# Performance work log

Measured on AMD Instinct MI355X. Metric: run time of the kernel, lower is better.

## Reference

```python
import jax, jax.numpy as jnp
import numpy as np


def _rnn_scan(x_tbi, h0, Wih, Whh, bih, bhh):
    # x_tbi: [T,B,I], h0: [B,H]. PyTorch nn.RNN cell: h = tanh(x@Wih^T + bih + h@Whh^T + bhh)
    def step(h, xt):
        h_new = jnp.tanh(xt @ Wih.T + bih + h @ Whh.T + bhh)
        return h_new, h_new
    h_last, hs = jax.lax.scan(step, h0, x_tbi)
    return h_last, hs


def setup_inputs() -> dict:
    key = jax.random.key(0)
    ks = jax.random.split(key, 12)
    B, T, I, H, O = 4096, 64, 3, 128, 3
    s = 1.0 / np.sqrt(H)
    d = {
        "x": jax.random.normal(ks[0], (B, T, I), dtype=jnp.float32),
        "enc_Wih": jax.random.uniform(ks[1], (H, I), jnp.float32, -s, s),
        "enc_Whh": jax.random.uniform(ks[2], (H, H), jnp.float32, -s, s),
        "enc_bih": jax.random.uniform(ks[3], (H,), jnp.float32, -s, s),
        "enc_bhh": jax.random.uniform(ks[4], (H,), jnp.float32, -s, s),
        "dec_Wih": jax.random.uniform(ks[5], (H, O), jnp.float32, -s, s),
        "dec_Whh": jax.random.uniform(ks[6], (H, H), jnp.float32, -s, s),
        "dec_bih": jax.random.uniform(ks[7], (H,), jnp.float32, -s, s),
        "dec_bhh": jax.random.uniform(ks[8], (H,), jnp.float32, -s, s),
        "fc_W": jax.random.uniform(ks[9], (O, H), jnp.float32, -s, s),
        "fc_b": jax.random.uniform(ks[10], (O,), jnp.float32, -s, s),
        "pred_len": 32,
    }
    return d


def reference(x, enc_Wih, enc_Whh, enc_bih, enc_bhh,
              dec_Wih, dec_Whh, dec_bih, dec_bhh, fc_W, fc_b, pred_len):
    B, T, _ = x.shape
    H = enc_Whh.shape[0]
    h0 = jnp.zeros((B, H), dtype=x.dtype)
    # Encoder over LOOK_BACK steps
    h, _ = _rnn_scan(jnp.swapaxes(x, 0, 1), h0, enc_Wih, enc_Whh, enc_bih, enc_bhh)
    dec_in0 = x[:, -1, :]  # [B,O]

    def step(carry, _):
        h, inp = carry
        h_new = jnp.tanh(inp @ dec_Wih.T + dec_bih + h @ dec_Whh.T + dec_bhh)
        pred = h_new @ fc_W.T + fc_b
        return (h_new, pred), pred

    _, preds = jax.lax.scan(step, (h, dec_in0), None, length=pred_len)
    out = jnp.swapaxes(preds, 0, 1)  # [B, pred_len, O]
    if pred_len == 1:
        return out[:, 0, :]
    return out
```

## Files before the change

### kernel.cpp

```cpp
#include <hip/hip_runtime.h>

typedef short short8 __attribute__((ext_vector_type(8)));
typedef float f32x4 __attribute__((ext_vector_type(4)));

#define H 128
#define NB 16
#define TSTEPS 64
#define PRED 32


static __device__ __forceinline__ unsigned short bf16_rne(float f) {
  unsigned u = __builtin_bit_cast(unsigned, f);
  u += 0x7fffu + ((u >> 16) & 1u);
  return (unsigned short)(u >> 16);
}
static __device__ __forceinline__ float bf16_f(unsigned short s) {
  unsigned u = ((unsigned)s) << 16;
  return __builtin_bit_cast(float, u);
}
static __device__ __forceinline__ float tanh_fast(float v) {
  v = fminf(9.0f, fmaxf(-9.0f, v));
  float e = __expf(2.0f * v);
  return __fdividef(e - 1.0f, e + 1.0f);
}

static __device__ __forceinline__ void split_frag(const f32x4& a, const f32x4& b,
                                                  short8& hi, short8& lo) {
  #pragma unroll
  for (int e = 0; e < 4; ++e) {
    unsigned short h1 = bf16_rne(a[e]);
    hi[e] = (short)h1;
    lo[e] = (short)bf16_rne(a[e] - bf16_f(h1));
    unsigned short h2 = bf16_rne(b[e]);
    hi[e + 4] = (short)h2;
    lo[e + 4] = (short)bf16_rne(b[e] - bf16_f(h2));
  }
}

__global__ __launch_bounds__(512, 2) void traj_kernel(
    const float* __restrict__ x,
    const float* __restrict__ eWih, const float* __restrict__ eWhh,
    const float* __restrict__ ebih, const float* __restrict__ ebhh,
    const float* __restrict__ dWih, const float* __restrict__ dWhh,
    const float* __restrict__ dbih, const float* __restrict__ dbhh,
    const float* __restrict__ fcW, const float* __restrict__ fcb,
    float* __restrict__ out)
{
  __shared__ __align__(16) short h_hi0[NB * H];
  __shared__ __align__(16) short h_hi1[NB * H];

  const int tid = threadIdx.x;
  const int lane = tid & 63;
  const int w = tid >> 6;
  const int l4 = lane >> 4;
  const int ln = lane & 15;
  const int r0 = blockIdx.x * NB;
  const int jj = w * 16 + ln;

  #pragma unroll
  for (int s = 0; s < 4; ++s)
    h_hi0[tid + s * 512] = 0;

  short8 whi[4], wlo[4];
  #pragma unroll
  for (int kt = 0; kt < 4; ++kt) {
    const float* p = eWhh + jj * H + kt * 32 + l4 * 8;
    split_frag(*(const f32x4*)p, *(const f32x4*)(p + 4), whi[kt], wlo[kt]);
  }
  float bias = ebih[jj] + ebhh[jj];
  float wi[3];
  #pragma unroll
  for (int i = 0; i < 3; ++i) wi[i] = eWih[jj * 3 + i];

  int roff[4];
  #pragma unroll
  for (int kt = 0; kt < 4; ++kt)
    roff[kt] = ln * H + ((((kt << 2) + l4) ^ ln) << 3);
  int wo[4];
  const float* xrow[4];
  #pragma unroll
  for (int reg = 0; reg < 4; ++reg) {
    const int r = l4 * 4 + reg;
    wo[reg] = r * H + (((jj >> 3) ^ r) << 3) + (jj & 7);
    xrow[reg] = x + (size_t)(r0 + r) * 192;
  }

  auto load_frags = [&](const short* __restrict__ hh, short8* ah) {
    #pragma unroll
    for (int kt = 0; kt < 4; ++kt)
      ah[kt] = *(const short8*)&hh[roff[kt]];
  };
  auto rnn_core = [&](const short8* ah, f32x4 acc0, short* __restrict__ wh) {
    f32x4 accb = {0.f, 0.f, 0.f, 0.f};
    #pragma unroll
    for (int kt = 0; kt < 4; ++kt) {
      acc0 = __builtin_amdgcn_mfma_f32_16x16x32_bf16(ah[kt], whi[kt], acc0, 0, 0, 0);
      accb = __builtin_amdgcn_mfma_f32_16x16x32_bf16(ah[kt], wlo[kt], accb, 0, 0, 0);
    }
    #pragma unroll
    for (int reg = 0; reg < 4; ++reg) {
      float v = tanh_fast(acc0[reg] + accb[reg]);
      wh[wo[reg]] = (short)bf16_rne(v);
    }
  };

  float xc[4][3], xn[4][3];
  #pragma unroll
  for (int reg = 0; reg < 4; ++reg)
    #pragma unroll
    for (int i = 0; i < 3; ++i) xc[reg][i] = xrow[reg][i];

  __syncthreads();

  for (int t = 0; t < TSTEPS; t += 2) {
    {
      short8 ah[4];
      load_frags(h_hi0, ah);
      f32x4 a;
      #pragma unroll
      for (int reg = 0; reg < 4; ++reg)
        a[reg] = bias + wi[0] * xc[reg][0] + wi[1] * xc[reg][1] + wi[2] * xc[reg][2];
      #pragma unroll
      for (int reg = 0; reg < 4; ++reg)
        #pragma unroll
        for (int i = 0; i < 3; ++i) xn[reg][i] = xrow[reg][(t + 1) * 3 + i];
      rnn_core(ah, a, h_hi1);
      __syncthreads();
    }
    {
      short8 ah[4];
      load_frags(h_hi1, ah);
      f32x4 a;
      #pragma unroll
      for (int reg = 0; reg < 4; ++reg)
        a[reg] = bias + wi[0] * xn[reg][0] + wi[1] * xn[reg][1] + wi[2] * xn[reg][2];
      const int tp = (t + 2 < TSTEPS) ? (t + 2) : (TSTEPS - 1);
      #pragma unroll
      for (int reg = 0; reg < 4; ++reg)
        #pragma unroll
        for (int i = 0; i < 3; ++i) xc[reg][i] = xrow[reg][tp * 3 + i];
      rnn_core(ah, a, h_hi0);
      __syncthreads();
    }
  }

  #pragma unroll
  for (int kt = 0; kt < 4; ++kt) {
    const float* p = dWhh + jj * H + kt * 32 + l4 * 8;
    split_frag(*(const f32x4*)p, *(const f32x4*)(p + 4), whi[kt], wlo[kt]);
  }
  bias = dbih[jj] + dbhh[jj];
  #pragma unroll
  for (int i = 0; i < 3; ++i) wi[i] = dWih[jj * 3 + i];

  short8 fhi[4];
  #pragma unroll
  for (int kt = 0; kt < 4; ++kt) {
    f32x4 a = {0.f, 0.f, 0.f, 0.f}, b = {0.f, 0.f, 0.f, 0.f};
    if (ln < 3) {
      const float* p = fcW + ln * H + kt * 32 + l4 * 8;
      a = *(const f32x4*)p;
      b = *(const f32x4*)(p + 4);
    }
    short8 hi;
    #pragma unroll
    for (int e = 0; e < 4; ++e) {
      hi[e] = (short)bf16_rne(a[e]);
      hi[e + 4] = (short)bf16_rne(b[e]);
    }
    fhi[kt] = hi;
  }
  const float fcbl = (ln < 3) ? fcb[ln] : 0.f;

  {
    short8 ah[4];
    load_frags(h_hi0, ah);
    f32x4 a;
    #pragma unroll
    for (int reg = 0; reg < 4; ++reg)
      a[reg] = bias + wi[0] * xc[reg][0] + wi[1] * xc[reg][1] + wi[2] * xc[reg][2];
    rnn_core(ah, a, h_hi1);
  }
  __syncthreads();

  #pragma unroll
  for (int kt = 0; kt < 4; ++kt) {
    const int kb = kt * 32 + l4 * 8;
    f32x4 a = *(const f32x4*)(dWhh + jj * H + kb);
    f32x4 b = *(const f32x4*)(dWhh + jj * H + kb + 4);
    #pragma unroll
    for (int o = 0; o < 3; ++o) {
      const f32x4 fa = *(const f32x4*)(fcW + o * H + kb);
      const f32x4 fb = *(const f32x4*)(fcW + o * H + kb + 4);
      #pragma unroll
      for (int e = 0; e < 4; ++e) {
        a[e] += wi[o] * fa[e];
        b[e] += wi[o] * fb[e];
      }
    }
    split_frag(a, b, whi[kt], wlo[kt]);
  }
  const float biasp = bias + wi[0] * fcb[0] + wi[1] * fcb[1] + wi[2] * fcb[2];
  const f32x4 accd = {biasp, biasp, biasp, biasp};

  const short* rdh = h_hi1;
  short* wrh = h_hi0;
  for (int s = 1; s < PRED; ++s) {
    short8 ah[4];
    load_frags(rdh, ah);
    rnn_core(ah, accd, wrh);
    if (w == (s & 7)) {
      f32x4 p0 = {0.f, 0.f, 0.f, 0.f};
      #pragma unroll
      for (int kt = 0; kt < 4; ++kt)
        p0 = __builtin_amdgcn_mfma_f32_16x16x32_bf16(ah[kt], fhi[kt], p0, 0, 0, 0);
      if (ln < 3) {
        #pragma unroll
        for (int reg = 0; reg < 4; ++reg)
          out[((size_t)(r0 + l4 * 4 + reg) * PRED + (s - 1)) * 3 + ln] =
              p0[reg] + fcbl;
      }
    }
    __syncthreads();
    const short* th = rdh; rdh = wrh; wrh = (short*)th;
  }
  if (w == 0) {
    short8 ah[4];
    load_frags(rdh, ah);
    f32x4 p0 = {0.f, 0.f, 0.f, 0.f};
    #pragma unroll
    for (int kt = 0; kt < 4; ++kt)
      p0 = __builtin_amdgcn_mfma_f32_16x16x32_bf16(ah[kt], fhi[kt], p0, 0, 0, 0);
    if (ln < 3) {
      #pragma unroll
      for (int reg = 0; reg < 4; ++reg)
        out[((size_t)(r0 + l4 * 4 + reg) * PRED + (PRED - 1)) * 3 + ln] =
            p0[reg] + fcbl;
    }
  }
}

extern "C" void kernel_launch(void* const* d_in, const int* in_sizes, int n_in,
                              void* d_out, int out_size, void* d_ws, size_t ws_size,
                              hipStream_t stream) {
  (void)in_sizes; (void)n_in; (void)out_size; (void)d_ws; (void)ws_size;
  const float* x    = (const float*)d_in[0];
  const float* eWih = (const float*)d_in[1];
  const float* eWhh = (const float*)d_in[2];
  const float* ebih = (const float*)d_in[3];
  const float* ebhh = (const float*)d_in[4];
  const float* dWih = (const float*)d_in[5];
  const float* dWhh = (const float*)d_in[6];
  const float* dbih = (const float*)d_in[7];
  const float* dbhh = (const float*)d_in[8];
  const float* fcW  = (const float*)d_in[9];
  const float* fcb  = (const float*)d_in[10];
  float* out = (float*)d_out;
  traj_kernel<<<dim3(256), dim3(512), 0, stream>>>(
      x, eWih, eWhh, ebih, ebhh, dWih, dWhh, dbih, dbhh, fcW, fcb, out);
}
```

Measured before the change: 136.9 us.

## Stage block's input sequence in LDS and move prediction stores past barrier

Each block now loads its whole 16x64x3 input slice into shared memory once, with coalesced reads, padded to 4 floats per timestep. Each encoder step then reads its inputs with a single vector LDS load instead of per-step scattered global loads that sat on the recurrent critical path. In the decoder, the global stores of predictions move after the barrier so they no longer delay the synchronisation. This adds about 16KB of LDS per block, which could lower occupancy at two blocks per CU.

```diff
diff --git a/kernel.cpp b/kernel.cpp
--- a/kernel.cpp
+++ b/kernel.cpp
@@ -7,6 +7,7 @@
 #define NB 16
 #define TSTEPS 64
 #define PRED 32
+#define XSTRIDE 260
 
 
 static __device__ __forceinline__ unsigned short bf16_rne(float f) {
@@ -46,6 +47,7 @@
     const float* __restrict__ fcW, const float* __restrict__ fcb,
     float* __restrict__ out)
 {
+  __shared__ __align__(16) float x_lds[NB * XSTRIDE];
   __shared__ __align__(16) short h_hi0[NB * H];
   __shared__ __align__(16) short h_hi1[NB * H];
 
@@ -58,6 +60,15 @@
   const int jj = w * 16 + ln;
 
   #pragma unroll
+  for (int s = 0; s < 6; ++s) {
+    int flat = tid + s * 512;
+    int r = flat / 192;
+    int rem = flat - r * 192;
+    int t = rem / 3;
+    int i = rem - t * 3;
+    x_lds[r * XSTRIDE + t * 4 + i] = x[(size_t)r0 * 192 + flat];
+  }
+  #pragma unroll
   for (int s = 0; s < 4; ++s)
     h_hi0[tid + s * 512] = 0;
 
@@ -76,13 +87,12 @@
   #pragma unroll
   for (int kt = 0; kt < 4; ++kt)
     roff[kt] = ln * H + ((((kt << 2) + l4) ^ ln) << 3);
-  int wo[4];
-  const float* xrow[4];
+  int wo[4], xb[4];
   #pragma unroll
   for (int reg = 0; reg < 4; ++reg) {
     const int r = l4 * 4 + reg;
     wo[reg] = r * H + (((jj >> 3) ^ r) << 3) + (jj & 7);
-    xrow[reg] = x + (size_t)(r0 + r) * 192;
+    xb[reg] = r * XSTRIDE;
   }
 
   auto load_frags = [&](const short* __restrict__ hh, short8* ah) {
@@ -104,12 +114,6 @@
     }
   };
 
-  float xc[4][3], xn[4][3];
-  #pragma unroll
-  for (int reg = 0; reg < 4; ++reg)
-    #pragma unroll
-    for (int i = 0; i < 3; ++i) xc[reg][i] = xrow[reg][i];
-
   __syncthreads();
 
   for (int t = 0; t < TSTEPS; t += 2) {
@@ -118,12 +122,10 @@
       load_frags(h_hi0, ah);
       f32x4 a;
       #pragma unroll
-      for (int reg = 0; reg < 4; ++reg)
-        a[reg] = bias + wi[0] * xc[reg][0] + wi[1] * xc[reg][1] + wi[2] * xc[reg][2];
-      #pragma unroll
-      for (int reg = 0; reg < 4; ++reg)
-        #pragma unroll
-        for (int i = 0; i < 3; ++i) xn[reg][i] = xrow[reg][(t + 1) * 3 + i];
+      for (int reg = 0; reg < 4; ++reg) {
+        const f32x4 xv = *(const f32x4*)&x_lds[xb[reg] + t * 4];
+        a[reg] = bias + wi[0] * xv[0] + wi[1] * xv[1] + wi[2] * xv[2];
+      }
       rnn_core(ah, a, h_hi1);
       __syncthreads();
     }
@@ -132,13 +134,10 @@
       load_frags(h_hi1, ah);
       f32x4 a;
       #pragma unroll
-      for (int reg = 0; reg < 4; ++reg)
-        a[reg] = bias + wi[0] * xn[reg][0] + wi[1] * xn[reg][1] + wi[2] * xn[reg][2];
-      const int tp = (t + 2 < TSTEPS) ? (t + 2) : (TSTEPS - 1);
-      #pragma unroll
-      for (int reg = 0; reg < 4; ++reg)
-        #pragma unroll
-        for (int i = 0; i < 3; ++i) xc[reg][i] = xrow[reg][tp * 3 + i];
+      for (int reg = 0; reg < 4; ++reg) {
+        const f32x4 xv = *(const f32x4*)&x_lds[xb[reg] + (t + 1) * 4];
+        a[reg] = bias + wi[0] * xv[0] + wi[1] * xv[1] + wi[2] * xv[2];
+      }
       rnn_core(ah, a, h_hi0);
       __syncthreads();
     }
@@ -177,8 +176,10 @@
     load_frags(h_hi0, ah);
     f32x4 a;
     #pragma unroll
-    for (int reg = 0; reg < 4; ++reg)
-      a[reg] = bias + wi[0] * xc[reg][0] + wi[1] * xc[reg][1] + wi[2] * xc[reg][2];
+    for (int reg = 0; reg < 4; ++reg) {
+      const f32x4 xv = *(const f32x4*)&x_lds[xb[reg] + 63 * 4];
+      a[reg] = bias + wi[0] * xv[0] + wi[1] * xv[1] + wi[2] * xv[2];
+    }
     rnn_core(ah, a, h_hi1);
   }
   __syncthreads();
@@ -209,19 +210,20 @@
     short8 ah[4];
     load_frags(rdh, ah);
     rnn_core(ah, accd, wrh);
-    if (w == (s & 7)) {
-      f32x4 p0 = {0.f, 0.f, 0.f, 0.f};
+    f32x4 p0 = {0.f, 0.f, 0.f, 0.f};
+    const bool mywave = (w == (s & 7));
+    if (mywave) {
       #pragma unroll
       for (int kt = 0; kt < 4; ++kt)
         p0 = __builtin_amdgcn_mfma_f32_16x16x32_bf16(ah[kt], fhi[kt], p0, 0, 0, 0);
-      if (ln < 3) {
-        #pragma unroll
-        for (int reg = 0; reg < 4; ++reg)
-          out[((size_t)(r0 + l4 * 4 + reg) * PRED + (s - 1)) * 3 + ln] =
-              p0[reg] + fcbl;
-      }
     }
     __syncthreads();
+    if (mywave && ln < 3) {
+      #pragma unroll
+      for (int reg = 0; reg < 4; ++reg)
+        out[((size_t)(r0 + l4 * 4 + reg) * PRED + (s - 1)) * 3 + ln] =
+            p0[reg] + fcbl;
+    }
     const short* th = rdh; rdh = wrh; wrh = (short*)th;
   }
   if (w == 0) {
```

After: 141.8 us. +3.5%, slower.
